# Optimization experiments

Measured on AMD Instinct MI355X. Metric: run time of the kernel, lower is better.

The kernel has to match this reference:

```python
import jax, jax.numpy as jnp
import numpy as np
from jax import lax

TOP_K = 4
ROUTED_SCALING = 1.0
RENORMALIZE = True


def setup_inputs() -> dict:
    key = jax.random.key(0)
    ks = jax.random.split(key, 9)
    H, I, E = 2048, 1024, 16
    s = 0.02
    return {
        "hidden_states": jax.random.normal(ks[0], (2, 1024, H), jnp.float32),
        "gate_w": jax.random.normal(ks[1], (E, H), jnp.float32) * s,
        "expert_bias": jax.random.normal(ks[2], (E,), jnp.float32) * s,
        "w_gate": jax.random.normal(ks[3], (E, I, H), jnp.float32) * s,
        "w_up": jax.random.normal(ks[4], (E, I, H), jnp.float32) * s,
        "w_down": jax.random.normal(ks[5], (E, H, I), jnp.float32) * s,
        "sw_gate": jax.random.normal(ks[6], (I, H), jnp.float32) * s,
        "sw_up": jax.random.normal(ks[7], (I, H), jnp.float32) * s,
        "sw_down": jax.random.normal(ks[8], (H, I), jnp.float32) * s,
    }


def _swiglu_ffn(x, wg, wu, wd):
    # SiluAndMul(gate_up) -> down_proj
    return (jax.nn.silu(x @ wg.T) * (x @ wu.T)) @ wd.T


def reference(hidden_states, gate_w, expert_bias, w_gate, w_up, w_down,
              sw_gate, sw_up, sw_down):
    orig_shape = hidden_states.shape
    H = orig_shape[-1]
    x = hidden_states.reshape(-1, H)            # [T, H]
    T = x.shape[0]

    # --- sigmoid gating with score-correction bias (bias affects selection only) ---
    logits = x.astype(jnp.float32) @ gate_w.T    # [T, E] fp32 router
    scores = jax.nn.sigmoid(logits)
    _, topk_idx = lax.top_k(scores + expert_bias[None, :], TOP_K)   # [T, K]
    topk_w = jnp.take_along_axis(scores, topk_idx, axis=-1)         # raw scores
    if RENORMALIZE:
        topk_w = topk_w / jnp.sum(topk_w, axis=-1, keepdims=True)
    topk_w = topk_w * ROUTED_SCALING

    # scatter top-k weights into dense [T, E] combine matrix
    E = gate_w.shape[0]
    combine = jnp.zeros((T, E), dtype=x.dtype).at[
        jnp.arange(T)[:, None], topk_idx].set(topk_w.astype(x.dtype))

    # --- routed experts: scan over experts, weighted accumulate ---
    def step(acc, ws):
        wg, wu, wd, cw = ws                     # cw: [T] combine weights
        return acc + cw[:, None] * _swiglu_ffn(x, wg, wu, wd), None

    routed, _ = lax.scan(step, jnp.zeros_like(x),
                         (w_gate, w_up, w_down, combine.T))

    # --- shared expert ---
    shared = _swiglu_ffn(x, sw_gate, sw_up, sw_down)

    return (routed + shared).reshape(orig_shape)
```

## Files before the change

kernel.cpp:

```cpp
#include <hip/hip_runtime.h>
#include <hip/hip_bf16.h>
#include <cstdint>

#define TK 2048
#define HD 2048
#define ID 1024
#define NE 16
#define NG 17
#define TOPK 4
#define SLOTS (TK*TOPK)
#define ROWS_ALL (SLOTS+TK)
#define IH (ID*HD)
#define MAXT 96

typedef __attribute__((ext_vector_type(4))) float f32x4;
typedef __attribute__((ext_vector_type(8))) short s16x8;
typedef unsigned short u16;
typedef unsigned long long u64;

__device__ __forceinline__ u16 f2bf(float f){
  union { float f; uint32_t u; } v; v.f = f;
  uint32_t r = v.u + 0x7fffu + ((v.u >> 16) & 1u);
  return (u16)(r >> 16);
}

#define GLD16(g, l) __builtin_amdgcn_global_load_lds( \
    (const __attribute__((address_space(1))) void*)(g), \
    (__attribute__((address_space(3))) void*)(l), 16, 0, 0)

__device__ __forceinline__ const s16x8* fragp(const u16* b, int row, int off){
  return (const s16x8*)((const char*)b + row*128 + (off ^ ((row&7)<<4)));
}

__global__ void k_prep(const float* __restrict__ x, u16* __restrict__ xb,
                       float* __restrict__ out, int out_n, u64* __restrict__ maskbits){
  int gi = blockIdx.x*blockDim.x + threadIdx.x;
  int st = gridDim.x*blockDim.x;
  if (gi < NE*32) maskbits[gi] = 0ull;
  for (int i=gi; i<out_n; i+=st) out[i] = 0.f;
  for (int i=gi; i<TK*HD/4; i+=st){
    float4 f = ((const float4*)x)[i];
    ushort4 o; o.x=f2bf(f.x); o.y=f2bf(f.y); o.z=f2bf(f.z); o.w=f2bf(f.w);
    ((ushort4*)xb)[i] = o;
  }
}

__global__ void k_cvtw(const float* __restrict__ wg, const float* __restrict__ wu,
                       const float* __restrict__ wd, const float* __restrict__ swg,
                       const float* __restrict__ swu, const float* __restrict__ swd,
                       u16* __restrict__ wgb, u16* __restrict__ wub, u16* __restrict__ wdb){
  const size_t nbig = (size_t)NE*IH/4, nsml = IH/4;
  const size_t total = 3*nbig + 3*nsml;
  for (size_t i = (size_t)blockIdx.x*blockDim.x + threadIdx.x; i < total;
       i += (size_t)gridDim.x*blockDim.x){
    const float4* src; ushort4* dst; size_t j = i;
    if (j < nbig){ src=(const float4*)wg + j;  dst=(ushort4*)wgb + j; }
    else if ((j-=nbig) < nbig){ src=(const float4*)wu + j;  dst=(ushort4*)wub + j; }
    else if ((j-=nbig) < nbig){ src=(const float4*)wd + j;  dst=(ushort4*)wdb + j; }
    else if ((j-=nbig) < nsml){ src=(const float4*)swg + j; dst=(ushort4*)wgb + nbig + j; }
    else if ((j-=nsml) < nsml){ src=(const float4*)swu + j; dst=(ushort4*)wub + nbig + j; }
    else { j-=nsml; src=(const float4*)swd + j; dst=(ushort4*)wdb + nbig + j; }
    float4 f = *src;
    ushort4 o; o.x=f2bf(f.x); o.y=f2bf(f.y); o.z=f2bf(f.z); o.w=f2bf(f.w);
    *dst = o;
  }
}

__global__ __launch_bounds__(256) void k_logits(const float* __restrict__ x,
                                                const float* __restrict__ gw,
                                                const float* __restrict__ bias,
                                                float* __restrict__ wdense,
                                                u64* __restrict__ maskbits){
  int t = blockIdx.x, tid = threadIdx.x;
  int lane = tid & 63, wv = tid >> 6;
  const float* xr = x + (size_t)t*HD;
  float acc[NE];
  #pragma unroll
  for (int e=0;e<NE;e++) acc[e]=0.f;
  for (int k=tid;k<HD;k+=256){
    float xv = xr[k];
    #pragma unroll
    for (int e=0;e<NE;e++) acc[e] += xv * gw[e*HD + k];
  }
  __shared__ float red[NE][4];
  #pragma unroll
  for (int e=0;e<NE;e++){
    float v = acc[e];
    #pragma unroll
    for (int off=32;off>0;off>>=1) v += __shfl_down(v, off, 64);
    if (lane==0) red[e][wv] = v;
  }
  __syncthreads();
  if (tid == 0){
    float sc[NE], bs[NE];
    #pragma unroll
    for (int e=0;e<NE;e++){
      float l = red[e][0]+red[e][1]+red[e][2]+red[e][3];
      float s = 1.f/(1.f+expf(-l));
      sc[e]=s; bs[e]=s+bias[e];
    }
    int idx[TOPK]; float wsum=0.f; unsigned used=0;
    for (int k=0;k<TOPK;k++){
      int best=0; float bv=-1e30f;
      for (int e=0;e<NE;e++) if (!((used>>e)&1u) && bs[e] > bv){ bv=bs[e]; best=e; }
      used |= 1u<<best; idx[k]=best; wsum += sc[best];
    }
    float inv = 1.f/wsum;
    for (int k=0;k<TOPK;k++){
      int e = idx[k];
      wdense[t*NE + e] = sc[e]*inv;
      atomicOr(&maskbits[e*32 + (t>>6)], 1ull << (t&63));
    }
  }
}

__global__ void k_scan(const u64* __restrict__ maskbits, int* __restrict__ counts,
                       int* __restrict__ offsets, int* __restrict__ wordpfx,
                       int* __restrict__ tiles){
  int acc = 0;
  for (int e=0;e<NE;e++){
    int c = 0;
    for (int w=0;w<32;w++){ wordpfx[e*32+w] = c; c += __popcll(maskbits[e*32+w]); }
    counts[e] = c;
  }
  for (int e=0;e<NE;e++){ offsets[e] = acc; acc += counts[e]; }
  offsets[NE] = acc;
  counts[NE] = TK;
  int nt = 0;
  for (int g=0; g<NG; g++){
    int c = counts[g];
    for (int mt=0; mt*128 < c && nt < MAXT; mt++) tiles[nt++] = (g<<8) | mt;
  }
  for (; nt<MAXT; nt++) tiles[nt] = -1;
}

__global__ void k_scatter(const u64* __restrict__ maskbits, const int* __restrict__ offsets,
                          const int* __restrict__ wordpfx, const float* __restrict__ wdense,
                          int* __restrict__ rowtok, float* __restrict__ roww){
  int t = blockIdx.x*blockDim.x + threadIdx.x;
  int e = blockIdx.y;
  if (t >= TK) return;
  if (e == NE){ rowtok[offsets[NE]+t] = t; roww[offsets[NE]+t] = 1.f; return; }
  u64 w = maskbits[e*32 + (t>>6)];
  if ((w >> (t&63)) & 1ull){
    int pos = offsets[e] + wordpfx[e*32 + (t>>6)] + __popcll(w & ((1ull << (t&63)) - 1ull));
    rowtok[pos] = t; roww[pos] = wdense[t*NE + e];
  }
}

__global__ __launch_bounds__(256) void k_gemm1b(
    const u16* __restrict__ xb, const u16* __restrict__ wgb, const u16* __restrict__ wub,
    const int* __restrict__ counts, const int* __restrict__ offsets,
    const int* __restrict__ rowtok, const float* __restrict__ roww,
    const int* __restrict__ tiles, u16* __restrict__ P)
{
  int te = tiles[blockIdx.y];
  if (te < 0) return;
  int g = te >> 8, mt = te & 255;
  int cnt = counts[g];
  int n0 = blockIdx.x*64;
  int base = offsets[g];
  const u16* wg16 = wgb + (size_t)g*IH;
  const u16* wu16 = wub + (size_t)g*IH;

  __shared__ u16 lsA[2][128*64];
  __shared__ u16 lsG[2][64*64];
  __shared__ u16 lsU[2][64*64];

  int tid = threadIdx.x, lane = tid & 63, wv = tid >> 6;
  int wm = (wv>>1)*64, wn = (wv&1)*32;
  int rl = lane & 15, hi = lane >> 4;

  f32x4 accg[4][2] = {}; f32x4 accu[4][2] = {};

  const u16* aSrc[4];
  #pragma unroll
  for (int i=0;i<4;i++){
    int b = i*256 + tid, r = b>>3, cb = b&7;
    int m = mt*128 + r; if (m >= cnt) m = cnt-1;
    int tok = rowtok[base + m];
    aSrc[i] = xb + (size_t)tok*HD + ((cb ^ (r&7))<<3);
  }
  const u16 *gSrc[2], *uSrc[2];
  #pragma unroll
  for (int i=0;i<2;i++){
    int b = i*256 + tid, r = b>>3, cb = b&7;
    size_t off = (size_t)(n0 + r)*HD + ((cb ^ (r&7))<<3);
    gSrc[i] = wg16 + off; uSrc[i] = wu16 + off;
  }

  #pragma unroll
  for (int i=0;i<4;i++) GLD16(aSrc[i], &lsA[0][(i*256 + wv*64)*8]);
  #pragma unroll
  for (int i=0;i<2;i++) GLD16(gSrc[i], &lsG[0][(i*256 + wv*64)*8]);
  #pragma unroll
  for (int i=0;i<2;i++) GLD16(uSrc[i], &lsU[0][(i*256 + wv*64)*8]);

  const int ntile = HD/64;
  for (int t=0; t<ntile; ++t){
    int cur = t & 1, nxt = cur ^ 1;
    bool more = (t+1 < ntile);
    if (more){
      int k1 = (t+1)*64;
      #pragma unroll
      for (int i=0;i<4;i++) GLD16(aSrc[i]+k1, &lsA[nxt][(i*256 + wv*64)*8]);
      #pragma unroll
      for (int i=0;i<2;i++) GLD16(gSrc[i]+k1, &lsG[nxt][(i*256 + wv*64)*8]);
      #pragma unroll
      for (int i=0;i<2;i++) GLD16(uSrc[i]+k1, &lsU[nxt][(i*256 + wv*64)*8]);
      asm volatile("s_waitcnt vmcnt(8)" ::: "memory");
    } else {
      asm volatile("s_waitcnt vmcnt(0)" ::: "memory");
    }
    __builtin_amdgcn_s_barrier();
    const u16* A = lsA[cur]; const u16* G = lsG[cur]; const u16* U = lsU[cur];
    #pragma unroll
    for (int ks=0; ks<2; ++ks){
      int off = ks*64 + hi*16;
      s16x8 af[4];
      #pragma unroll
      for (int mi=0;mi<4;mi++) af[mi] = *fragp(A, wm+16*mi+rl, off);
      #pragma unroll
      for (int ni=0;ni<2;ni++){
        s16x8 bg = *fragp(G, wn+16*ni+rl, off);
        s16x8 bu = *fragp(U, wn+16*ni+rl, off);
        #pragma unroll
        for (int mi=0;mi<4;mi++){
          accg[mi][ni] = __builtin_amdgcn_mfma_f32_16x16x32_bf16(af[mi], bg, accg[mi][ni], 0,0,0);
          accu[mi][ni] = __builtin_amdgcn_mfma_f32_16x16x32_bf16(af[mi], bu, accu[mi][ni], 0,0,0);
        }
      }
    }
    asm volatile("s_waitcnt lgkmcnt(0)" ::: "memory");
    __builtin_amdgcn_s_barrier();
  }
  int rl4 = hi*4, cl = rl;
  #pragma unroll
  for (int mi=0;mi<4;mi++){
    #pragma unroll
    for (int j=0;j<4;j++){
      int m = mt*128 + wm + mi*16 + rl4 + j;
      if (m < cnt){
        int slot = base + m;
        float wgt = roww[slot];
        #pragma unroll
        for (int ni=0;ni<2;ni++){
          float gv = accg[mi][ni][j], uv = accu[mi][ni][j];
          float pv = gv/(1.f+expf(-gv))*uv*wgt;
          P[(size_t)slot*ID + n0 + wn + ni*16 + cl] = f2bf(pv);
        }
      }
    }
  }
}

__global__ __launch_bounds__(256) void k_gemm2b(
    const u16* __restrict__ P, const u16* __restrict__ wdb,
    const int* __restrict__ counts, const int* __restrict__ offsets,
    const int* __restrict__ rowtok, const int* __restrict__ tiles,
    float* __restrict__ out)
{
  int te = tiles[blockIdx.y];
  if (te < 0) return;
  int g = te >> 8, mt = te & 255;
  int cnt = counts[g];
  int n0 = blockIdx.x*128;
  int base = offsets[g];
  const u16* wd16 = wdb + (size_t)g*IH;

  __shared__ u16 lsA[2][128*64];
  __shared__ u16 lsB[2][128*64];

  int tid = threadIdx.x, lane = tid & 63, wv = tid >> 6;
  int wm = (wv>>1)*64, wn = (wv&1)*64;
  int rl = lane & 15, hi = lane >> 4;
  f32x4 acc[4][4] = {};

  const u16 *aSrc[4], *bSrc[4];
  #pragma unroll
  for (int i=0;i<4;i++){
    int b = i*256 + tid, r = b>>3, cb = b&7;
    int m = mt*128 + r; if (m >= cnt) m = cnt-1;
    aSrc[i] = P + (size_t)(base + m)*ID + ((cb ^ (r&7))<<3);
    bSrc[i] = wd16 + (size_t)(n0 + r)*ID + ((cb ^ (r&7))<<3);
  }

  #pragma unroll
  for (int i=0;i<4;i++) GLD16(aSrc[i], &lsA[0][(i*256 + wv*64)*8]);
  #pragma unroll
  for (int i=0;i<4;i++) GLD16(bSrc[i], &lsB[0][(i*256 + wv*64)*8]);

  const int ntile = ID/64;
  for (int t=0; t<ntile; ++t){
    int cur = t & 1, nxt = cur ^ 1;
    bool more = (t+1 < ntile);
    if (more){
      int k1 = (t+1)*64;
      #pragma unroll
      for (int i=0;i<4;i++) GLD16(aSrc[i]+k1, &lsA[nxt][(i*256 + wv*64)*8]);
      #pragma unroll
      for (int i=0;i<4;i++) GLD16(bSrc[i]+k1, &lsB[nxt][(i*256 + wv*64)*8]);
      asm volatile("s_waitcnt vmcnt(8)" ::: "memory");
    } else {
      asm volatile("s_waitcnt vmcnt(0)" ::: "memory");
    }
    __builtin_amdgcn_s_barrier();
    const u16* A = lsA[cur]; const u16* B = lsB[cur];
    #pragma unroll
    for (int ks=0; ks<2; ++ks){
      int off = ks*64 + hi*16;
      s16x8 af[4], bf[4];
      #pragma unroll
      for (int mi=0;mi<4;mi++) af[mi] = *fragp(A, wm+16*mi+rl, off);
      #pragma unroll
      for (int ni=0;ni<4;ni++) bf[ni] = *fragp(B, wn+16*ni+rl, off);
      #pragma unroll
      for (int mi=0;mi<4;mi++)
        #pragma unroll
        for (int ni=0;ni<4;ni++)
          acc[mi][ni] = __builtin_amdgcn_mfma_f32_16x16x32_bf16(af[mi], bf[ni], acc[mi][ni], 0,0,0);
    }
    asm volatile("s_waitcnt lgkmcnt(0)" ::: "memory");
    __builtin_amdgcn_s_barrier();
  }
  int rl4 = hi*4, cl = rl;
  #pragma unroll
  for (int mi=0;mi<4;mi++){
    #pragma unroll
    for (int j=0;j<4;j++){
      int m = mt*128 + wm + mi*16 + rl4 + j;
      if (m < cnt){
        int tok = rowtok[base + m];
        #pragma unroll
        for (int ni=0;ni<4;ni++)
          atomicAdd(&out[(size_t)tok*HD + n0 + wn + ni*16 + cl], acc[mi][ni][j]);
      }
    }
  }
}


extern "C" void kernel_launch(void* const* d_in, const int* in_sizes, int n_in,
                              void* d_out, int out_size, void* d_ws, size_t ws_size,
                              hipStream_t stream){
  (void)in_sizes; (void)n_in; (void)ws_size;
  const float* x       = (const float*)d_in[0];
  const float* gate_w  = (const float*)d_in[1];
  const float* ebias   = (const float*)d_in[2];
  const float* w_gate  = (const float*)d_in[3];
  const float* w_up    = (const float*)d_in[4];
  const float* w_down  = (const float*)d_in[5];
  const float* sw_gate = (const float*)d_in[6];
  const float* sw_up   = (const float*)d_in[7];
  const float* sw_down = (const float*)d_in[8];
  float* out = (float*)d_out;

  char* p = (char*)d_ws;
  auto alloc = [&](size_t bytes)->char*{ char* r = p; p += (bytes + 255) & ~(size_t)255; return r; };
  u16*   xb       = (u16*)  alloc((size_t)TK*HD*2);
  u16*   P        = (u16*)  alloc((size_t)ROWS_ALL*ID*2);
  float* wdense   = (float*)alloc((size_t)TK*NE*4);
  u64*   maskbits = (u64*)  alloc((size_t)NE*32*8);
  int*   wordpfx  = (int*)  alloc((size_t)NE*32*4);
  int*   counts   = (int*)  alloc(64);
  int*   offsets  = (int*)  alloc(64);
  int*   tiles    = (int*)  alloc(MAXT*4);
  int*   rowtok   = (int*)  alloc((size_t)ROWS_ALL*4);
  float* roww     = (float*)alloc((size_t)ROWS_ALL*4);
  size_t slab = (size_t)NG*IH*2;
  u16* wgb = (u16*)alloc(slab);
  u16* wub = (u16*)alloc(slab);
  u16* wdb = (u16*)alloc(slab);

  k_prep<<<2048, 256, 0, stream>>>(x, xb, out, out_size, maskbits);
  k_cvtw<<<2048, 256, 0, stream>>>(w_gate, w_up, w_down, sw_gate, sw_up, sw_down,
                                   wgb, wub, wdb);
  k_logits<<<TK, 256, 0, stream>>>(x, gate_w, ebias, wdense, maskbits);
  k_scan<<<1, 1, 0, stream>>>(maskbits, counts, offsets, wordpfx, tiles);
  k_scatter<<<dim3(TK/256, NG), 256, 0, stream>>>(maskbits, offsets, wordpfx, wdense, rowtok, roww);

  dim3 g1(ID/64, MAXT);
  dim3 g2(HD/128, MAXT);
  k_gemm1b<<<g1, 256, 0, stream>>>(xb, wgb, wub, counts, offsets, rowtok, roww, tiles, P);
  k_gemm2b<<<g2, 256, 0, stream>>>(P, wdb, counts, offsets, rowtok, tiles, out);
}
```

Baseline: 440.8 us.

## Use 32x32 MFMA with larger tiles and plain-store shared expert down-proj

Both grouped GEMMs move from 16x16x32 to 32x32x16 bf16 MFMA with larger N tiles (128 for gate/up, 256 for down) and launch_bounds(256,2). Double-buffered LDS is replaced by a single buffer with a full vmcnt(0) wait each k-step. The shared-expert down projection now runs first as a separate pass that writes output with plain stores. This replaces the output zeroing in k_prep and the atomics for the shared rows. Routed tiles then atomically add on top, which relies on stream ordering and removes overlap of loads with compute.

```diff
diff --git a/kernel.cpp b/kernel.cpp
--- a/kernel.cpp
+++ b/kernel.cpp
@@ -12,8 +12,10 @@
 #define ROWS_ALL (SLOTS+TK)
 #define IH (ID*HD)
 #define MAXT 96
+#define MAXTR 80
 
 typedef __attribute__((ext_vector_type(4))) float f32x4;
+typedef __attribute__((ext_vector_type(16))) float f32x16;
 typedef __attribute__((ext_vector_type(8))) short s16x8;
 typedef unsigned short u16;
 typedef unsigned long long u64;
@@ -32,12 +34,13 @@
   return (const s16x8*)((const char*)b + row*128 + (off ^ ((row&7)<<4)));
 }
 
+#define MFMA32(a,b,c) __builtin_amdgcn_mfma_f32_32x32x16_bf16((a),(b),(c),0,0,0)
+
 __global__ void k_prep(const float* __restrict__ x, u16* __restrict__ xb,
-                       float* __restrict__ out, int out_n, u64* __restrict__ maskbits){
+                       u64* __restrict__ maskbits){
   int gi = blockIdx.x*blockDim.x + threadIdx.x;
   int st = gridDim.x*blockDim.x;
   if (gi < NE*32) maskbits[gi] = 0ull;
-  for (int i=gi; i<out_n; i+=st) out[i] = 0.f;
   for (int i=gi; i<TK*HD/4; i+=st){
     float4 f = ((const float4*)x)[i];
     ushort4 o; o.x=f2bf(f.x); o.y=f2bf(f.y); o.z=f2bf(f.z); o.w=f2bf(f.w);
@@ -116,7 +119,7 @@
 
 __global__ void k_scan(const u64* __restrict__ maskbits, int* __restrict__ counts,
                        int* __restrict__ offsets, int* __restrict__ wordpfx,
-                       int* __restrict__ tiles){
+                       int* __restrict__ tiles, int* __restrict__ tilesR){
   int acc = 0;
   for (int e=0;e<NE;e++){
     int c = 0;
@@ -126,12 +129,16 @@
   for (int e=0;e<NE;e++){ offsets[e] = acc; acc += counts[e]; }
   offsets[NE] = acc;
   counts[NE] = TK;
-  int nt = 0;
+  int nt = 0, nr = 0;
   for (int g=0; g<NG; g++){
     int c = counts[g];
-    for (int mt=0; mt*128 < c && nt < MAXT; mt++) tiles[nt++] = (g<<8) | mt;
-  }
-  for (; nt<MAXT; nt++) tiles[nt] = -1;
+    for (int mt=0; mt*128 < c; mt++){
+      if (nt < MAXT) tiles[nt++] = (g<<8) | mt;
+      if (g < NE && nr < MAXTR) tilesR[nr++] = (g<<8) | mt;
+    }
+  }
+  for (; nt<MAXT;  nt++) tiles[nt]  = -1;
+  for (; nr<MAXTR; nr++) tilesR[nr] = -1;
 }
 
 __global__ void k_scatter(const u64* __restrict__ maskbits, const int* __restrict__ offsets,
@@ -148,7 +155,7 @@
   }
 }
 
-__global__ __launch_bounds__(256) void k_gemm1b(
+__global__ __launch_bounds__(256, 2) void k_gemm1b(
     const u16* __restrict__ xb, const u16* __restrict__ wgb, const u16* __restrict__ wub,
     const int* __restrict__ counts, const int* __restrict__ offsets,
     const int* __restrict__ rowtok, const float* __restrict__ roww,
@@ -158,182 +165,163 @@
   if (te < 0) return;
   int g = te >> 8, mt = te & 255;
   int cnt = counts[g];
-  int n0 = blockIdx.x*64;
+  int n0 = blockIdx.x*128;
   int base = offsets[g];
   const u16* wg16 = wgb + (size_t)g*IH;
   const u16* wu16 = wub + (size_t)g*IH;
 
-  __shared__ u16 lsA[2][128*64];
-  __shared__ u16 lsG[2][64*64];
-  __shared__ u16 lsU[2][64*64];
+  __shared__ u16 lsA[128*64];
+  __shared__ u16 lsG[128*64];
+  __shared__ u16 lsU[128*64];
 
   int tid = threadIdx.x, lane = tid & 63, wv = tid >> 6;
-  int wm = (wv>>1)*64, wn = (wv&1)*32;
-  int rl = lane & 15, hi = lane >> 4;
-
-  f32x4 accg[4][2] = {}; f32x4 accu[4][2] = {};
-
-  const u16* aSrc[4];
+  int wm = (wv>>1)*64, wn64 = (wv&1)*64;
+  int rl = lane & 31, hi = lane >> 5;
+
+  f32x16 accg[2][2] = {}; f32x16 accu[2][2] = {};
+
+  const u16 *aSrc[4], *gSrc[4], *uSrc[4];
   #pragma unroll
   for (int i=0;i<4;i++){
     int b = i*256 + tid, r = b>>3, cb = b&7;
     int m = mt*128 + r; if (m >= cnt) m = cnt-1;
     int tok = rowtok[base + m];
     aSrc[i] = xb + (size_t)tok*HD + ((cb ^ (r&7))<<3);
-  }
-  const u16 *gSrc[2], *uSrc[2];
-  #pragma unroll
-  for (int i=0;i<2;i++){
-    int b = i*256 + tid, r = b>>3, cb = b&7;
-    size_t off = (size_t)(n0 + r)*HD + ((cb ^ (r&7))<<3);
-    gSrc[i] = wg16 + off; uSrc[i] = wu16 + off;
-  }
-
-  #pragma unroll
-  for (int i=0;i<4;i++) GLD16(aSrc[i], &lsA[0][(i*256 + wv*64)*8]);
-  #pragma unroll
-  for (int i=0;i<2;i++) GLD16(gSrc[i], &lsG[0][(i*256 + wv*64)*8]);
-  #pragma unroll
-  for (int i=0;i<2;i++) GLD16(uSrc[i], &lsU[0][(i*256 + wv*64)*8]);
-
-  const int ntile = HD/64;
-  for (int t=0; t<ntile; ++t){
-    int cur = t & 1, nxt = cur ^ 1;
-    bool more = (t+1 < ntile);
-    if (more){
-      int k1 = (t+1)*64;
+    size_t woff = (size_t)(n0 + r)*HD + ((cb ^ (r&7))<<3);
+    gSrc[i] = wg16 + woff; uSrc[i] = wu16 + woff;
+  }
+
+  for (int t=0; t<HD/64; ++t){
+    int k0 = t*64;
+    #pragma unroll
+    for (int i=0;i<4;i++) GLD16(aSrc[i]+k0, lsA + (i*256 + wv*64)*8);
+    #pragma unroll
+    for (int i=0;i<4;i++) GLD16(gSrc[i]+k0, lsG + (i*256 + wv*64)*8);
+    #pragma unroll
+    for (int i=0;i<4;i++) GLD16(uSrc[i]+k0, lsU + (i*256 + wv*64)*8);
+    asm volatile("s_waitcnt vmcnt(0)" ::: "memory");
+    __builtin_amdgcn_s_barrier();
+    #pragma unroll
+    for (int s=0; s<4; ++s){
+      int off = s*32 + hi*16;
+      s16x8 af[2], bg[2], bu[2];
+      af[0] = *fragp(lsA, wm + rl, off);
+      af[1] = *fragp(lsA, wm + 32 + rl, off);
+      bg[0] = *fragp(lsG, wn64 + rl, off);
+      bg[1] = *fragp(lsG, wn64 + 32 + rl, off);
+      bu[0] = *fragp(lsU, wn64 + rl, off);
+      bu[1] = *fragp(lsU, wn64 + 32 + rl, off);
       #pragma unroll
-      for (int i=0;i<4;i++) GLD16(aSrc[i]+k1, &lsA[nxt][(i*256 + wv*64)*8]);
-      #pragma unroll
-      for (int i=0;i<2;i++) GLD16(gSrc[i]+k1, &lsG[nxt][(i*256 + wv*64)*8]);
-      #pragma unroll
-      for (int i=0;i<2;i++) GLD16(uSrc[i]+k1, &lsU[nxt][(i*256 + wv*64)*8]);
-      asm volatile("s_waitcnt vmcnt(8)" ::: "memory");
-    } else {
-      asm volatile("s_waitcnt vmcnt(0)" ::: "memory");
-    }
-    __builtin_amdgcn_s_barrier();
-    const u16* A = lsA[cur]; const u16* G = lsG[cur]; const u16* U = lsU[cur];
-    #pragma unroll
-    for (int ks=0; ks<2; ++ks){
-      int off = ks*64 + hi*16;
-      s16x8 af[4];
-      #pragma unroll
-      for (int mi=0;mi<4;mi++) af[mi] = *fragp(A, wm+16*mi+rl, off);
-      #pragma unroll
-      for (int ni=0;ni<2;ni++){
-        s16x8 bg = *fragp(G, wn+16*ni+rl, off);
-        s16x8 bu = *fragp(U, wn+16*ni+rl, off);
+      for (int mi=0;mi<2;mi++){
         #pragma unroll
-        for (int mi=0;mi<4;mi++){
-          accg[mi][ni] = __builtin_amdgcn_mfma_f32_16x16x32_bf16(af[mi], bg, accg[mi][ni], 0,0,0);
-          accu[mi][ni] = __builtin_amdgcn_mfma_f32_16x16x32_bf16(af[mi], bu, accu[mi][ni], 0,0,0);
+        for (int j=0;j<2;j++){
+          accg[mi][j] = MFMA32(af[mi], bg[j], accg[mi][j]);
+          accu[mi][j] = MFMA32(af[mi], bu[j], accu[mi][j]);
         }
       }
     }
     asm volatile("s_waitcnt lgkmcnt(0)" ::: "memory");
     __builtin_amdgcn_s_barrier();
   }
-  int rl4 = hi*4, cl = rl;
-  #pragma unroll
-  for (int mi=0;mi<4;mi++){
-    #pragma unroll
-    for (int j=0;j<4;j++){
-      int m = mt*128 + wm + mi*16 + rl4 + j;
+  #pragma unroll
+  for (int mi=0;mi<2;mi++){
+    #pragma unroll
+    for (int r=0;r<16;r++){
+      int rowb = wm + mi*32 + (r&3) + 8*(r>>2) + 4*hi;
+      int m = mt*128 + rowb;
       if (m < cnt){
         int slot = base + m;
         float wgt = roww[slot];
         #pragma unroll
-        for (int ni=0;ni<2;ni++){
-          float gv = accg[mi][ni][j], uv = accu[mi][ni][j];
+        for (int j=0;j<2;j++){
+          float gv = accg[mi][j][r], uv = accu[mi][j][r];
           float pv = gv/(1.f+expf(-gv))*uv*wgt;
-          P[(size_t)slot*ID + n0 + wn + ni*16 + cl] = f2bf(pv);
+          P[(size_t)slot*ID + n0 + wn64 + j*32 + rl] = f2bf(pv);
         }
       }
     }
   }
 }
 
-__global__ __launch_bounds__(256) void k_gemm2b(
+template<bool ATOMIC>
+__global__ __launch_bounds__(256, 2) void k_gemm2b(
     const u16* __restrict__ P, const u16* __restrict__ wdb,
     const int* __restrict__ counts, const int* __restrict__ offsets,
     const int* __restrict__ rowtok, const int* __restrict__ tiles,
     float* __restrict__ out)
 {
-  int te = tiles[blockIdx.y];
-  if (te < 0) return;
-  int g = te >> 8, mt = te & 255;
-  int cnt = counts[g];
-  int n0 = blockIdx.x*128;
-  int base = offsets[g];
+  int g, mt, cnt, base;
+  if (ATOMIC){
+    int te = tiles[blockIdx.y];
+    if (te < 0) return;
+    g = te >> 8; mt = te & 255; cnt = counts[g]; base = offsets[g];
+  } else {
+    g = NE; mt = blockIdx.y; cnt = TK; base = SLOTS;
+  }
+  int n0 = blockIdx.x*256;
   const u16* wd16 = wdb + (size_t)g*IH;
 
-  __shared__ u16 lsA[2][128*64];
-  __shared__ u16 lsB[2][128*64];
+  __shared__ u16 lsA[128*64];
+  __shared__ u16 lsB[256*64];
 
   int tid = threadIdx.x, lane = tid & 63, wv = tid >> 6;
-  int wm = (wv>>1)*64, wn = (wv&1)*64;
-  int rl = lane & 15, hi = lane >> 4;
-  f32x4 acc[4][4] = {};
-
-  const u16 *aSrc[4], *bSrc[4];
+  int wm = (wv>>1)*64, wn = (wv&1)*128;
+  int rl = lane & 31, hi = lane >> 5;
+  f32x16 acc[2][4] = {};
+
+  const u16* aSrc[4];
   #pragma unroll
   for (int i=0;i<4;i++){
     int b = i*256 + tid, r = b>>3, cb = b&7;
     int m = mt*128 + r; if (m >= cnt) m = cnt-1;
     aSrc[i] = P + (size_t)(base + m)*ID + ((cb ^ (r&7))<<3);
+  }
+  const u16* bSrc[8];
+  #pragma unroll
+  for (int i=0;i<8;i++){
+    int b = i*256 + tid, r = b>>3, cb = b&7;
     bSrc[i] = wd16 + (size_t)(n0 + r)*ID + ((cb ^ (r&7))<<3);
   }
 
-  #pragma unroll
-  for (int i=0;i<4;i++) GLD16(aSrc[i], &lsA[0][(i*256 + wv*64)*8]);
-  #pragma unroll
-  for (int i=0;i<4;i++) GLD16(bSrc[i], &lsB[0][(i*256 + wv*64)*8]);
-
-  const int ntile = ID/64;
-  for (int t=0; t<ntile; ++t){
-    int cur = t & 1, nxt = cur ^ 1;
-    bool more = (t+1 < ntile);
-    if (more){
-      int k1 = (t+1)*64;
+  for (int t=0; t<ID/64; ++t){
+    int k0 = t*64;
+    #pragma unroll
+    for (int i=0;i<4;i++) GLD16(aSrc[i]+k0, lsA + (i*256 + wv*64)*8);
+    #pragma unroll
+    for (int i=0;i<8;i++) GLD16(bSrc[i]+k0, lsB + (i*256 + wv*64)*8);
+    asm volatile("s_waitcnt vmcnt(0)" ::: "memory");
+    __builtin_amdgcn_s_barrier();
+    #pragma unroll
+    for (int s=0; s<4; ++s){
+      int off = s*32 + hi*16;
+      s16x8 af[2], bf[4];
+      af[0] = *fragp(lsA, wm + rl, off);
+      af[1] = *fragp(lsA, wm + 32 + rl, off);
       #pragma unroll
-      for (int i=0;i<4;i++) GLD16(aSrc[i]+k1, &lsA[nxt][(i*256 + wv*64)*8]);
+      for (int nj=0;nj<4;nj++) bf[nj] = *fragp(lsB, wn + nj*32 + rl, off);
       #pragma unroll
-      for (int i=0;i<4;i++) GLD16(bSrc[i]+k1, &lsB[nxt][(i*256 + wv*64)*8]);
-      asm volatile("s_waitcnt vmcnt(8)" ::: "memory");
-    } else {
-      asm volatile("s_waitcnt vmcnt(0)" ::: "memory");
-    }
-    __builtin_amdgcn_s_barrier();
-    const u16* A = lsA[cur]; const u16* B = lsB[cur];
-    #pragma unroll
-    for (int ks=0; ks<2; ++ks){
-      int off = ks*64 + hi*16;
-      s16x8 af[4], bf[4];
-      #pragma unroll
-      for (int mi=0;mi<4;mi++) af[mi] = *fragp(A, wm+16*mi+rl, off);
-      #pragma unroll
-      for (int ni=0;ni<4;ni++) bf[ni] = *fragp(B, wn+16*ni+rl, off);
-      #pragma unroll
-      for (int mi=0;mi<4;mi++)
+      for (int mi=0;mi<2;mi++)
         #pragma unroll
-        for (int ni=0;ni<4;ni++)
-          acc[mi][ni] = __builtin_amdgcn_mfma_f32_16x16x32_bf16(af[mi], bf[ni], acc[mi][ni], 0,0,0);
+        for (int nj=0;nj<4;nj++)
+          acc[mi][nj] = MFMA32(af[mi], bf[nj], acc[mi][nj]);
     }
     asm volatile("s_waitcnt lgkmcnt(0)" ::: "memory");
     __builtin_amdgcn_s_barrier();
   }
-  int rl4 = hi*4, cl = rl;
-  #pragma unroll
-  for (int mi=0;mi<4;mi++){
-    #pragma unroll
-    for (int j=0;j<4;j++){
-      int m = mt*128 + wm + mi*16 + rl4 + j;
+  #pragma unroll
+  for (int mi=0;mi<2;mi++){
+    #pragma unroll
+    for (int r=0;r<16;r++){
+      int rowb = wm + mi*32 + (r&3) + 8*(r>>2) + 4*hi;
+      int m = mt*128 + rowb;
       if (m < cnt){
         int tok = rowtok[base + m];
+        float* orow = out + (size_t)tok*HD + n0 + wn + rl;
         #pragma unroll
-        for (int ni=0;ni<4;ni++)
-          atomicAdd(&out[(size_t)tok*HD + n0 + wn + ni*16 + cl], acc[mi][ni][j]);
+        for (int nj=0;nj<4;nj++){
+          if (ATOMIC) atomicAdd(orow + nj*32, acc[mi][nj][r]);
+          else        orow[nj*32] = acc[mi][nj][r];
+        }
       }
     }
   }
@@ -343,7 +331,7 @@
 extern "C" void kernel_launch(void* const* d_in, const int* in_sizes, int n_in,
                               void* d_out, int out_size, void* d_ws, size_t ws_size,
                               hipStream_t stream){
-  (void)in_sizes; (void)n_in; (void)ws_size;
+  (void)in_sizes; (void)n_in; (void)ws_size; (void)out_size;
   const float* x       = (const float*)d_in[0];
   const float* gate_w  = (const float*)d_in[1];
   const float* ebias   = (const float*)d_in[2];
@@ -365,6 +353,7 @@
   int*   counts   = (int*)  alloc(64);
   int*   offsets  = (int*)  alloc(64);
   int*   tiles    = (int*)  alloc(MAXT*4);
+  int*   tilesR   = (int*)  alloc(MAXTR*4);
   int*   rowtok   = (int*)  alloc((size_t)ROWS_ALL*4);
   float* roww     = (float*)alloc((size_t)ROWS_ALL*4);
   size_t slab = (size_t)NG*IH*2;
@@ -372,15 +361,17 @@
   u16* wub = (u16*)alloc(slab);
   u16* wdb = (u16*)alloc(slab);
 
-  k_prep<<<2048, 256, 0, stream>>>(x, xb, out, out_size, maskbits);
+  k_prep<<<2048, 256, 0, stream>>>(x, xb, maskbits);
   k_cvtw<<<2048, 256, 0, stream>>>(w_gate, w_up, w_down, sw_gate, sw_up, sw_down,
                                    wgb, wub, wdb);
   k_logits<<<TK, 256, 0, stream>>>(x, gate_w, ebias, wdense, maskbits);
-  k_scan<<<1, 1, 0, stream>>>(maskbits, counts, offsets, wordpfx, tiles);
+  k_scan<<<1, 1, 0, stream>>>(maskbits, counts, offsets, wordpfx, tiles, tilesR);
   k_scatter<<<dim3(TK/256, NG), 256, 0, stream>>>(maskbits, offsets, wordpfx, wdense, rowtok, roww);
 
-  dim3 g1(ID/64, MAXT);
-  dim3 g2(HD/128, MAXT);
+  dim3 g1(ID/128, MAXT);
   k_gemm1b<<<g1, 256, 0, stream>>>(xb, wgb, wub, counts, offsets, rowtok, roww, tiles, P);
-  k_gemm2b<<<g2, 256, 0, stream>>>(P, wdb, counts, offsets, rowtok, tiles, out);
-}
+  dim3 g2s(HD/256, TK/128);
+  k_gemm2b<false><<<g2s, 256, 0, stream>>>(P, wdb, counts, offsets, rowtok, nullptr, out);
+  dim3 g2r(HD/256, MAXTR);
+  k_gemm2b<true ><<<g2r, 256, 0, stream>>>(P, wdb, counts, offsets, rowtok, tilesR, out);
+}
```

Result: slower. 461.5 us (+4.7%).
